# Optimization experiments

Measured on AMD Instinct MI355X. Metric: run time of the kernel, lower is better.

## Reference

```python
import jax, jax.numpy as jnp
import numpy as np

N_VARS = 50_000
N_CLAUSES = 210_000
NNZ = 3 * N_CLAUSES
F = 80
NORM_EPS = 1e-3


def setup_inputs() -> dict:
    key = jax.random.key(0)
    ks = jax.random.split(key, 16)

    def w(k, fan_in, shape):
        return jax.random.normal(k, shape, jnp.float32) * (1.0 / np.sqrt(fan_in))

    inp = {
        'edge_lit': jax.random.randint(ks[0], (NNZ,), 0, 2 * N_VARS, jnp.int32),
        'edge_clause': jnp.sort(jax.random.randint(ks[1], (NNZ,), 0, N_CLAUSES, jnp.int32)),
        'n_vars': N_VARS,
        'n_clauses': N_CLAUSES,
        'L_init_scale': jnp.full((1,), 1.0 / np.sqrt(F), jnp.float32),
        'C_init_scale': jnp.full((1,), 1.0 / np.sqrt(F), jnp.float32),
        'LC_scale': jnp.full((1,), 0.1, jnp.float32),
        'CL_scale': jnp.full((1,), 0.1, jnp.float32),
        # C_update MLP: 160 -> 160 (relu6) -> 80
        'Cw1': w(ks[2], 160, (160, 160)), 'Cb1': jnp.zeros((160,), jnp.float32),
        'Cw2': w(ks[3], 160, (160, 80)), 'Cb2': jnp.zeros((80,), jnp.float32),
        # L_update MLP: 240 -> 240 (relu6) -> 80
        'Lw1': w(ks[4], 240, (240, 240)), 'Lb1': jnp.zeros((240,), jnp.float32),
        'Lw2': w(ks[5], 240, (240, 80)), 'Lb2': jnp.zeros((80,), jnp.float32),
        # V_score MLP: 160 -> 160 -> 160 -> 160 (relu6) -> 1
        'Vw1': w(ks[6], 160, (160, 160)), 'Vb1': jnp.zeros((160,), jnp.float32),
        'Vw2': w(ks[7], 160, (160, 160)), 'Vb2': jnp.zeros((160,), jnp.float32),
        'Vw3': w(ks[8], 160, (160, 160)), 'Vb3': jnp.zeros((160,), jnp.float32),
        'Vw4': w(ks[9], 160, (160, 1)), 'Vb4': jnp.zeros((1,), jnp.float32),
    }
    return inp


def _relu6(x):
    return jnp.minimum(jax.nn.relu(x), 6.0)


def _normalize(x):
    # tf.nn.moments over axis 0 (biased variance) + batch_normalization, no scale/offset
    m = jnp.mean(x, axis=0, keepdims=True)
    v = jnp.var(x, axis=0, keepdims=True)
    return (x - m) / jnp.sqrt(v + NORM_EPS)


def reference(edge_lit, edge_clause, n_vars, n_clauses,
              L_init_scale, C_init_scale, LC_scale, CL_scale,
              Cw1, Cb1, Cw2, Cb2, Lw1, Lb1, Lw2, Lb2,
              Vw1, Vb1, Vw2, Vb2, Vw3, Vb3, Vw4, Vb4):
    n_lits = 2 * n_vars
    L = jnp.ones((n_lits, F), jnp.float32) * L_init_scale
    C = jnp.ones((n_clauses, F), jnp.float32) * C_init_scale

    for _ in range(4):
        # SpMM: adj[n_lits, n_clauses]^T @ L via gather + segment_sum
        LC_msgs = jax.ops.segment_sum(L[edge_lit], edge_clause, num_segments=n_clauses) * LC_scale
        C = _relu6(jnp.concatenate([C, LC_msgs], axis=-1) @ Cw1 + Cb1) @ Cw2 + Cb2
        C = _normalize(C)
        CL_msgs = jax.ops.segment_sum(C[edge_clause], edge_lit, num_segments=n_lits) * CL_scale
        L_flip = jnp.concatenate([L[n_vars:], L[:n_vars]], axis=0)
        L = _relu6(jnp.concatenate([L, CL_msgs, L_flip], axis=-1) @ Lw1 + Lb1) @ Lw2 + Lb2
        L = _normalize(L)

    V = jnp.concatenate([L[:n_vars], L[n_vars:]], axis=1)  # [n_vars, 160]
    h = _relu6(V @ Vw1 + Vb1)
    h = _relu6(h @ Vw2 + Vb2)
    h = _relu6(h @ Vw3 + Vb3)
    V_scores = h @ Vw4 + Vb4  # [n_vars, 1]

    # softplus mixed loss over clauses (edge list encodes signed literals)
    sign = jnp.where(edge_lit < n_vars, 1.0, -1.0).astype(jnp.float32)
    var_idx = jnp.where(edge_lit < n_vars, edge_lit, edge_lit - n_vars)
    lit_vals = V_scores[var_idx, 0] * sign
    clause_sum = jax.ops.segment_sum(jax.nn.softplus(lit_vals), edge_clause, num_segments=n_clauses)
    clauses_val = jnp.exp(-clause_sum)
    logits_loss = jnp.sum(clauses_val * (-jnp.log(1.0 - clauses_val + 1e-8)))
    return V_scores, logits_loss
```

## Files before the change

kernel.cpp:

```cpp
#include <hip/hip_runtime.h>
#include <hip/hip_bf16.h>

#define NV 50000
#define NL 100000
#define NC 210000
#define NNZE 630000
#define F 80

#define TBM 192
#define TBN 80
#define TBK 32
#define LDA 40

#define FBM 128
#define CH 80
#define CHP 96
#define LDH 104

typedef unsigned short us;
typedef __attribute__((ext_vector_type(8))) short s8v;
typedef __attribute__((ext_vector_type(4))) float f4v;
typedef __attribute__((ext_vector_type(4))) unsigned short us4;
typedef __attribute__((ext_vector_type(8))) unsigned short us8;

__device__ inline us bf16_hi(float x) {
    return (us)(__builtin_bit_cast(unsigned int, x) >> 16);
}
__device__ inline float b2f(us h) {
    return __builtin_bit_cast(float, (unsigned int)h << 16);
}

__global__ void build_off(const int* __restrict__ ec, int* __restrict__ off,
                          int nnz, int nc) {
    int e = blockIdx.x * 256 + threadIdx.x;
    if (e >= nnz) return;
    int c = ec[e];
    if (e == 0) {
        for (int cc = 0; cc <= c; ++cc) off[cc] = 0;
    } else {
        int cp = ec[e - 1];
        for (int cc = cp + 1; cc <= c; ++cc) off[cc] = e;
    }
    if (e == nnz - 1) {
        for (int cc = c + 1; cc <= nc; ++cc) off[cc] = nnz;
    }
}

__global__ void fill_val(float* __restrict__ p, int n, const float* __restrict__ v) {
    int i = blockIdx.x * 256 + threadIdx.x;
    if (i < n) p[i] = v[0];
}
__global__ void zero_int(int* __restrict__ p, int n) {
    int i = blockIdx.x * 256 + threadIdx.x;
    if (i < n) p[i] = 0;
}

__global__ void hist_lit(const int* __restrict__ el, int* __restrict__ cnt) {
    int e = blockIdx.x * 256 + threadIdx.x;
    if (e < NNZE) atomicAdd(&cnt[el[e]], 1);
}

__global__ __launch_bounds__(256)
void scan1(const int* __restrict__ cnt, int* __restrict__ bsum, int n) {
    __shared__ int sd[256];
    int i = blockIdx.x * 256 + threadIdx.x;
    sd[threadIdx.x] = (i < n) ? cnt[i] : 0;
    __syncthreads();
    for (int k = 128; k; k >>= 1) {
        if (threadIdx.x < k) sd[threadIdx.x] += sd[threadIdx.x + k];
        __syncthreads();
    }
    if (threadIdx.x == 0) bsum[blockIdx.x] = sd[0];
}

__global__ __launch_bounds__(512)
void scan2(int* __restrict__ bsum, int nb) {
    __shared__ int sd[512];
    int t = threadIdx.x;
    sd[t] = (t < nb) ? bsum[t] : 0;
    __syncthreads();
    for (int off = 1; off < 512; off <<= 1) {
        int v = (t >= off) ? sd[t - off] : 0;
        __syncthreads();
        sd[t] += v;
        __syncthreads();
    }
    if (t < nb) bsum[t] = sd[t];
}

__global__ __launch_bounds__(256)
void scan3(const int* __restrict__ cnt, const int* __restrict__ bsum,
           int* __restrict__ loff, int n) {
    __shared__ int sd[256];
    int t = threadIdx.x;
    int i = blockIdx.x * 256 + t;
    int v = (i < n) ? cnt[i] : 0;
    sd[t] = v;
    __syncthreads();
    for (int off = 1; off < 256; off <<= 1) {
        int u = (t >= off) ? sd[t - off] : 0;
        __syncthreads();
        sd[t] += u;
        __syncthreads();
    }
    int base = blockIdx.x ? bsum[blockIdx.x - 1] : 0;
    if (i < n) loff[i] = base + sd[t] - v;
    if (i == n - 1) loff[n] = base + sd[t];
}

__global__ void scatter_lit(const int* __restrict__ el, const int* __restrict__ ec,
                            const int* __restrict__ loff, int* __restrict__ cur,
                            int* __restrict__ litc) {
    int e = blockIdx.x * 256 + threadIdx.x;
    if (e >= NNZE) return;
    int l = el[e];
    int pos = loff[l] + atomicAdd(&cur[l], 1);
    litc[pos] = ec[e];
}

__global__ void seg_sort(const int* __restrict__ loff, int* __restrict__ litc) {
    int l = blockIdx.x * 256 + threadIdx.x;
    if (l >= NL) return;
    int a = loff[l], b = loff[l + 1];
    for (int i = a + 1; i < b; ++i) {
        int key = litc[i];
        int j = i - 1;
        while (j >= a && litc[j] > key) { litc[j + 1] = litc[j]; --j; }
        litc[j + 1] = key;
    }
}

__global__ void split_w(const float* __restrict__ W, int K, int N,
                        us* __restrict__ Wh, us* __restrict__ Wl) {
    int idx = blockIdx.x * 256 + threadIdx.x;
    if (idx >= K * N) return;
    int k = idx / N, n = idx % N;
    float x = W[idx];
    us h = bf16_hi(x);
    Wh[(size_t)n * K + k] = h;
    Wl[(size_t)n * K + k] = bf16_hi(x - b2f(h));
}

__global__ void lc_gather(const float* __restrict__ L, const int* __restrict__ el,
                          const int* __restrict__ off, const float* __restrict__ scale,
                          float* __restrict__ LC) {
    int idx = blockIdx.x * 256 + threadIdx.x;
    if (idx >= NC * 20) return;
    int c = idx / 20, f4 = idx % 20;
    int e0 = off[c], e1 = off[c + 1];
    float4 s = make_float4(0.f, 0.f, 0.f, 0.f);
    for (int e = e0; e < e1; ++e) {
        const float4 v = *(const float4*)&L[(size_t)el[e] * F + f4 * 4];
        s.x += v.x; s.y += v.y; s.z += v.z; s.w += v.w;
    }
    float sc = scale[0];
    s.x *= sc; s.y *= sc; s.z *= sc; s.w *= sc;
    *(float4*)&LC[(size_t)c * F + f4 * 4] = s;
}

__global__ void cl_gather(const float* __restrict__ C, const int* __restrict__ loff,
                          const int* __restrict__ litc, const float* __restrict__ scale,
                          const float* __restrict__ statsC, float* __restrict__ CL) {
    int idx = blockIdx.x * 256 + threadIdx.x;
    if (idx >= NL * 20) return;
    int lit = idx / 20, f4 = idx % 20;
    int e0 = loff[lit], e1 = loff[lit + 1];
    float4 s = make_float4(0.f, 0.f, 0.f, 0.f);
    for (int e = e0; e < e1; ++e) {
        const float4 v = *(const float4*)&C[(size_t)litc[e] * F + f4 * 4];
        s.x += v.x; s.y += v.y; s.z += v.z; s.w += v.w;
    }
    float sc = scale[0];
    float cnt = (float)(e1 - e0);
    float r[4] = {s.x, s.y, s.z, s.w};
    float4 o;
#pragma unroll
    for (int j = 0; j < 4; ++j) {
        int col = f4 * 4 + j;
        float m = statsC[col], rs = statsC[80 + col];
        r[j] = (r[j] - cnt * m) * rs * sc;
    }
    o.x = r[0]; o.y = r[1]; o.z = r[2]; o.w = r[3];
    *(float4*)&CL[(size_t)lit * F + f4 * 4] = o;
}

__global__ __launch_bounds__(256, 2)
void mlp_fused(const float* __restrict__ A0, const float* __restrict__ A1,
               const float* __restrict__ A2, int pw, int flip2, int rbase,
               int M, int K1, int N1,
               const us* __restrict__ W1h, const us* __restrict__ W1l,
               const float* __restrict__ b1,
               const us* __restrict__ W2h, const us* __restrict__ W2l,
               const float* __restrict__ b2,
               float* __restrict__ Out, const float* __restrict__ nstat,
               float* __restrict__ Psum, float* __restrict__ Psq) {
    __shared__ __align__(16) us AsH[FBM * LDA];
    __shared__ __align__(16) us AsL[FBM * LDA];
    __shared__ __align__(16) us HsH[FBM * LDH];
    __shared__ __align__(16) us HsL[FBM * LDH];
    __shared__ float ns[160];
    __shared__ float bs1[240];
    __shared__ float csum[80], csq[80];

    const int t = threadIdx.x;
    const int m0 = blockIdx.x * FBM;
    const int w = t >> 6;
    const int l = t & 63;
    const int lr = l & 15;
    const int lk = (l >> 4) * 8;
    const int q = t & 3;
    const int rb = t >> 2;

    if (nstat && t < 160) ns[t] = nstat[t];
    if (t < N1) bs1[t] = b1[t];
    if (t < 80) { csum[t] = 0.f; csq[t] = 0.f; }
    for (int u = t; u < FBM * 4; u += 256) {
        int row = u >> 2, cq = u & 3;
        us4 z = {0, 0, 0, 0};
        *(us4*)&HsH[row * LDH + CH + cq * 4] = z;
        *(us4*)&HsL[row * LDH + CH + cq * 4] = z;
    }
    __syncthreads();

    f4v acc2[2][5];
#pragma unroll
    for (int i = 0; i < 2; ++i)
#pragma unroll
        for (int j = 0; j < 5; ++j) acc2[i][j] = (f4v)0.f;

    float4 pa[2][2];

#define ALOAD(K0)                                                              \
    {                                                                          \
        _Pragma("unroll")                                                      \
        for (int i = 0; i < 2; ++i) {                                          \
            int row = m0 + i * 64 + rb;                                        \
            int kg = (K0) + q * 8;                                             \
            float4 z = make_float4(0.f, 0.f, 0.f, 0.f);                        \
            pa[i][0] = z; pa[i][1] = z;                                        \
            if (row < M && kg < K1) {                                          \
                int piece = (kg >= pw) + (kg >= 2 * pw);                       \
                int kk = kg - piece * pw;                                      \
                const float* P = piece == 0 ? A0 : piece == 1 ? A1 : A2;       \
                int re = row;                                                  \
                if (piece == 2 && flip2) {                                     \
                    int g = rbase + row;                                       \
                    re = (g < NV) ? g + NV : g - NV;                           \
                }                                                              \
                const float* src = P + (size_t)re * pw + kk;                   \
                pa[i][0] = *(const float4*)src;                                \
                pa[i][1] = *(const float4*)(src + 4);                          \
                if (piece == 0 && nstat) {                                     \
                    float* pf = (float*)&pa[i][0];                             \
                    _Pragma("unroll")                                          \
                    for (int j = 0; j < 8; ++j)                                \
                        pf[j] = (pf[j] - ns[kk + j]) * ns[80 + kk + j];        \
                }                                                              \
            }                                                                  \
        }                                                                      \
    }

    const int nk1 = (K1 + TBK - 1) / TBK;

    for (int c2 = 0; c2 < N1; c2 += CH) {
        f4v acc1[5][2];
#pragma unroll
        for (int i = 0; i < 5; ++i)
#pragma unroll
            for (int j = 0; j < 2; ++j) acc1[i][j] = (f4v)0.f;

        ALOAD(0);
        for (int s = 0; s < nk1; ++s) {
            const int k0 = s * TBK;
#pragma unroll
            for (int i = 0; i < 2; ++i) {
                float f0[8] = {pa[i][0].x, pa[i][0].y, pa[i][0].z, pa[i][0].w,
                               pa[i][1].x, pa[i][1].y, pa[i][1].z, pa[i][1].w};
                us8 hv, lv;
#pragma unroll
                for (int j = 0; j < 8; ++j) {
                    us h = bf16_hi(f0[j]);
                    hv[j] = h;
                    lv[j] = bf16_hi(f0[j] - b2f(h));
                }
                int r = i * 64 + rb;
                *(us8*)&AsH[r * LDA + q * 8] = hv;
                *(us8*)&AsL[r * LDA + q * 8] = lv;
            }
            __syncthreads();

            s8v aH[2], aL[2], wH[5], wL[5];
#pragma unroll
            for (int mf = 0; mf < 2; ++mf) {
                int ar = w * 32 + mf * 16 + lr;
                aH[mf] = *(const s8v*)&AsH[ar * LDA + lk];
                aL[mf] = *(const s8v*)&AsL[ar * LDA + lk];
            }
            {
                int kg = k0 + lk;
                bool kv = kg < K1;
#pragma unroll
                for (int nf = 0; nf < 5; ++nf) {
                    int br = c2 + nf * 16 + lr;
                    s8v z = {0, 0, 0, 0, 0, 0, 0, 0};
                    wH[nf] = kv ? *(const s8v*)&W1h[(size_t)br * K1 + kg] : z;
                    wL[nf] = kv ? *(const s8v*)&W1l[(size_t)br * K1 + kg] : z;
                }
            }
            if (s + 1 < nk1) ALOAD(k0 + TBK);
#pragma unroll
            for (int nf = 0; nf < 5; ++nf)
#pragma unroll
                for (int mf = 0; mf < 2; ++mf) {
                    acc1[nf][mf] = __builtin_amdgcn_mfma_f32_16x16x32_bf16(wH[nf], aH[mf], acc1[nf][mf], 0, 0, 0);
                    acc1[nf][mf] = __builtin_amdgcn_mfma_f32_16x16x32_bf16(wL[nf], aH[mf], acc1[nf][mf], 0, 0, 0);
                    acc1[nf][mf] = __builtin_amdgcn_mfma_f32_16x16x32_bf16(wH[nf], aL[mf], acc1[nf][mf], 0, 0, 0);
                }
            __syncthreads();
        }

#pragma unroll
        for (int nf = 0; nf < 5; ++nf) {
            int n1b = nf * 16 + ((l >> 4) << 2);
#pragma unroll
            for (int mf = 0; mf < 2; ++mf) {
                int m = w * 32 + mf * 16 + lr;
                us4 hv, lv;
#pragma unroll
                for (int r = 0; r < 4; ++r) {
                    float v = acc1[nf][mf][r] + bs1[c2 + n1b + r];
                    v = fminf(fmaxf(v, 0.f), 6.f);
                    us h = bf16_hi(v);
                    hv[r] = h;
                    lv[r] = bf16_hi(v - b2f(h));
                }
                *(us4*)&HsH[m * LDH + n1b] = hv;
                *(us4*)&HsL[m * LDH + n1b] = lv;
            }
        }
        __syncthreads();

#pragma unroll
        for (int ks = 0; ks < 3; ++ks) {
            int klocal = ks * 32 + lk;
            s8v a2H[2], a2L[2], b2H[5], b2L[5];
#pragma unroll
            for (int mf = 0; mf < 2; ++mf) {
                int ar = w * 32 + mf * 16 + lr;
                a2H[mf] = *(const s8v*)&HsH[ar * LDH + klocal];
                a2L[mf] = *(const s8v*)&HsL[ar * LDH + klocal];
            }
            bool bval = klocal < CH;
            int kg = c2 + klocal;
#pragma unroll
            for (int nf = 0; nf < 5; ++nf) {
                int n2 = nf * 16 + lr;
                s8v z = {0, 0, 0, 0, 0, 0, 0, 0};
                b2H[nf] = bval ? *(const s8v*)&W2h[(size_t)n2 * N1 + kg] : z;
                b2L[nf] = bval ? *(const s8v*)&W2l[(size_t)n2 * N1 + kg] : z;
            }
#pragma unroll
            for (int mf = 0; mf < 2; ++mf)
#pragma unroll
                for (int nf = 0; nf < 5; ++nf) {
                    acc2[mf][nf] = __builtin_amdgcn_mfma_f32_16x16x32_bf16(a2H[mf], b2H[nf], acc2[mf][nf], 0, 0, 0);
                    acc2[mf][nf] = __builtin_amdgcn_mfma_f32_16x16x32_bf16(a2L[mf], b2H[nf], acc2[mf][nf], 0, 0, 0);
                    acc2[mf][nf] = __builtin_amdgcn_mfma_f32_16x16x32_bf16(a2H[mf], b2L[nf], acc2[mf][nf], 0, 0, 0);
                }
        }
        __syncthreads();
    }
#undef ALOAD

#pragma unroll
    for (int nf = 0; nf < 5; ++nf) {
        int col = nf * 16 + lr;
        float bv = b2[col];
        float ls = 0.f, lq = 0.f;
#pragma unroll
        for (int mf = 0; mf < 2; ++mf) {
            int rowb = m0 + w * 32 + mf * 16 + (l >> 4) * 4;
#pragma unroll
            for (int r = 0; r < 4; ++r) {
                int row = rowb + r;
                if (row < M) {
                    float v = acc2[mf][nf][r] + bv;
                    Out[(size_t)row * 80 + col] = v;
                    ls += v; lq += v * v;
                }
            }
        }
        ls += __shfl_xor(ls, 16); ls += __shfl_xor(ls, 32);
        lq += __shfl_xor(lq, 16); lq += __shfl_xor(lq, 32);
        if (l < 16) {
            atomicAdd(&csum[col], ls);
            atomicAdd(&csq[col], lq);
        }
    }
    __syncthreads();
    if (t < 80) {
        size_t pb = (size_t)blockIdx.x * 80 + t;
        Psum[pb] = csum[t];
        Psq[pb] = csq[t];
    }
}

__global__ __launch_bounds__(256, 3)
void gemm_mfma(const float* __restrict__ A0, const float* __restrict__ A1,
               const float* __restrict__ A2, int pw, int flip2, int rbase,
               int M, int K, int N,
               const us* __restrict__ Wh, const us* __restrict__ Wl,
               const float* __restrict__ bias, float* __restrict__ Out, int act) {
    __shared__ __align__(16) us AsH[TBM * LDA];
    __shared__ __align__(16) us AsL[TBM * LDA];
    __shared__ __align__(16) us BsH[TBN * LDA];
    __shared__ __align__(16) us BsL[TBN * LDA];

    const int t = threadIdx.x;
    const int m0 = blockIdx.x * TBM;
    const int n0 = blockIdx.y * TBN;
    const int w = t >> 6;
    const int l = t & 63;
    const int lr = l & 15;
    const int lk = (l >> 4) * 8;
    const int q = t & 3;
    const int rb = t >> 2;

    f4v acc[3][5];
#pragma unroll
    for (int i = 0; i < 3; ++i)
#pragma unroll
        for (int j = 0; j < 5; ++j) acc[i][j] = (f4v)0.f;

    float4 pa[3][2];

#define ALOAD(K0)                                                              \
    {                                                                          \
        _Pragma("unroll")                                                      \
        for (int i = 0; i < 3; ++i) {                                          \
            int row = m0 + i * 64 + rb;                                        \
            int kg = (K0) + q * 8;                                             \
            float4 z = make_float4(0.f, 0.f, 0.f, 0.f);                        \
            pa[i][0] = z; pa[i][1] = z;                                        \
            if (row < M && kg < K) {                                           \
                int piece = (kg >= pw) + (kg >= 2 * pw);                       \
                int kk = kg - piece * pw;                                      \
                const float* P = piece == 0 ? A0 : piece == 1 ? A1 : A2;       \
                int re = row;                                                  \
                if (piece == 2 && flip2) {                                     \
                    int g = rbase + row;                                       \
                    re = (g < NV) ? g + NV : g - NV;                           \
                }                                                              \
                const float* src = P + (size_t)re * pw + kk;                   \
                pa[i][0] = *(const float4*)src;                                \
                pa[i][1] = *(const float4*)(src + 4);                          \
            }                                                                  \
        }                                                                      \
    }

    const int nk = (K + TBK - 1) / TBK;
    ALOAD(0);

    for (int s = 0; s < nk; ++s) {
        const int k0 = s * TBK;
#pragma unroll
        for (int i = 0; i < 3; ++i) {
            float f0[8] = {pa[i][0].x, pa[i][0].y, pa[i][0].z, pa[i][0].w,
                           pa[i][1].x, pa[i][1].y, pa[i][1].z, pa[i][1].w};
            us8 hv, lv;
#pragma unroll
            for (int j = 0; j < 8; ++j) {
                us h = bf16_hi(f0[j]);
                hv[j] = h;
                lv[j] = bf16_hi(f0[j] - b2f(h));
            }
            int r = i * 64 + rb;
            *(us8*)&AsH[r * LDA + q * 8] = hv;
            *(us8*)&AsL[r * LDA + q * 8] = lv;
        }
#pragma unroll
        for (int i = 0; i < 3; ++i) {
            int u = i * 256 + t;
            if (u < 640) {
                int hi = (u < 320);
                int c = hi ? u : u - 320;
                int n = c >> 2, cq = c & 3;
                int kg = k0 + cq * 8;
                us8 v = {0, 0, 0, 0, 0, 0, 0, 0};
                if (kg < K)
                    v = *(const us8*)&(hi ? Wh : Wl)[(size_t)(n0 + n) * K + kg];
                *(us8*)&(hi ? BsH : BsL)[n * LDA + cq * 8] = v;
            }
        }
        __syncthreads();

        s8v aH[3], aL[3], bH[5], bL[5];
#pragma unroll
        for (int mf = 0; mf < 3; ++mf) {
            int ar = w * 48 + mf * 16 + lr;
            aH[mf] = *(const s8v*)&AsH[ar * LDA + lk];
            aL[mf] = *(const s8v*)&AsL[ar * LDA + lk];
        }
#pragma unroll
        for (int nf = 0; nf < 5; ++nf) {
            int br = nf * 16 + lr;
            bH[nf] = *(const s8v*)&BsH[br * LDA + lk];
            bL[nf] = *(const s8v*)&BsL[br * LDA + lk];
        }
        if (s + 1 < nk) ALOAD(k0 + TBK);
#pragma unroll
        for (int mf = 0; mf < 3; ++mf)
#pragma unroll
            for (int nf = 0; nf < 5; ++nf) {
                acc[mf][nf] = __builtin_amdgcn_mfma_f32_16x16x32_bf16(aH[mf], bH[nf], acc[mf][nf], 0, 0, 0);
                acc[mf][nf] = __builtin_amdgcn_mfma_f32_16x16x32_bf16(aL[mf], bH[nf], acc[mf][nf], 0, 0, 0);
                acc[mf][nf] = __builtin_amdgcn_mfma_f32_16x16x32_bf16(aH[mf], bL[nf], acc[mf][nf], 0, 0, 0);
            }
        __syncthreads();
    }
#undef ALOAD

#pragma unroll
    for (int mf = 0; mf < 3; ++mf) {
        int rowb = m0 + w * 48 + mf * 16 + (l >> 4) * 4;
#pragma unroll
        for (int nf = 0; nf < 5; ++nf) {
            int col = n0 + nf * 16 + lr;
            float bv = bias[col];
#pragma unroll
            for (int r = 0; r < 4; ++r) {
                int row = rowb + r;
                if (row < M) {
                    float v = acc[mf][nf][r] + bv;
                    if (act) v = fminf(fmaxf(v, 0.f), 6.f);
                    Out[(size_t)row * N + col] = v;
                }
            }
        }
    }
}

__global__ __launch_bounds__(256)
void colstats_final(const float* __restrict__ Psum, const float* __restrict__ Psq,
                    int nblk, int M, float* __restrict__ stats) {
    __shared__ float sd[256], qd[256];
    int c = blockIdx.x;
    int tid = threadIdx.x;
    float s = 0.f, q = 0.f;
    for (int b = tid; b < nblk; b += 256) {
        s += Psum[(size_t)b * 80 + c];
        q += Psq [(size_t)b * 80 + c];
    }
    sd[tid] = s; qd[tid] = q;
    __syncthreads();
    for (int k = 128; k; k >>= 1) {
        if (tid < k) { sd[tid] += sd[tid + k]; qd[tid] += qd[tid + k]; }
        __syncthreads();
    }
    if (tid == 0) {
        float mean = sd[0] / (float)M;
        float var = qd[0] / (float)M - mean * mean;
        if (var < 0.f) var = 0.f;
        stats[c] = mean;
        stats[80 + c] = rsqrtf(var + 1e-3f);
    }
}

__global__ void norm_apply(float* __restrict__ X, int M, const float* __restrict__ stats) {
    int idx = blockIdx.x * 256 + threadIdx.x;
    if (idx >= M * F) return;
    int c = idx % F;
    X[idx] = (X[idx] - stats[c]) * stats[80 + c];
}

__global__ __launch_bounds__(256)
void vscore_kernel(const float* __restrict__ H, const float* __restrict__ w,
                   const float* __restrict__ b, float* __restrict__ out, int M) {
    int wid = (blockIdx.x * 256 + threadIdx.x) / 64;
    int lane = threadIdx.x % 64;
    if (wid >= M) return;
    const float* row = H + (size_t)wid * 160;
    float s = 0.f;
    for (int c = lane; c < 160; c += 64) s += row[c] * w[c];
    for (int off = 32; off; off >>= 1) s += __shfl_down(s, off);
    if (lane == 0) out[wid] = s + b[0];
}

__global__ __launch_bounds__(256)
void loss_clause(const int* __restrict__ el, const int* __restrict__ off,
                 const float* __restrict__ scores, float* __restrict__ partial, int nc) {
    __shared__ float sd[256];
    int c = blockIdx.x * 256 + threadIdx.x;
    float term = 0.f;
    if (c < nc) {
        int e0 = off[c], e1 = off[c + 1];
        float cs = 0.f;
        for (int e = e0; e < e1; ++e) {
            int lit = el[e];
            float v = (lit < NV) ? scores[lit] : -scores[lit - NV];
            cs += fmaxf(v, 0.f) + log1pf(expf(-fabsf(v)));
        }
        float cv = expf(-cs);
        term = cv * (-logf(1.0f - cv + 1e-8f));
    }
    sd[threadIdx.x] = term;
    __syncthreads();
    for (int s = 128; s; s >>= 1) {
        if (threadIdx.x < s) sd[threadIdx.x] += sd[threadIdx.x + s];
        __syncthreads();
    }
    if (threadIdx.x == 0) partial[blockIdx.x] = sd[0];
}

__global__ void loss_final(const float* __restrict__ partial, int n, float* __restrict__ out) {
    __shared__ float sd[256];
    float s = 0.f;
    for (int i = threadIdx.x; i < n; i += 256) s += partial[i];
    sd[threadIdx.x] = s;
    __syncthreads();
    for (int k = 128; k; k >>= 1) {
        if (threadIdx.x < k) sd[threadIdx.x] += sd[threadIdx.x + k];
        __syncthreads();
    }
    if (threadIdx.x == 0) out[0] = sd[0];
}

static inline size_t alignup(size_t x) { return (x + 255) & ~(size_t)255; }

extern "C" void kernel_launch(void* const* d_in, const int* in_sizes, int n_in,
                              void* d_out, int out_size, void* d_ws, size_t ws_size,
                              hipStream_t stream) {
    const int*   el   = (const int*)d_in[0];
    const int*   ec   = (const int*)d_in[1];
    const float* l_init = (const float*)d_in[4];
    const float* c_init = (const float*)d_in[5];
    const float* lc_s = (const float*)d_in[6];
    const float* cl_s = (const float*)d_in[7];
    const float* Cw1 = (const float*)d_in[8],  *Cb1 = (const float*)d_in[9];
    const float* Cw2 = (const float*)d_in[10], *Cb2 = (const float*)d_in[11];
    const float* Lw1 = (const float*)d_in[12], *Lb1 = (const float*)d_in[13];
    const float* Lw2 = (const float*)d_in[14], *Lb2 = (const float*)d_in[15];
    const float* Vw1 = (const float*)d_in[16], *Vb1 = (const float*)d_in[17];
    const float* Vw2 = (const float*)d_in[18], *Vb2 = (const float*)d_in[19];
    const float* Vw3 = (const float*)d_in[20], *Vb3 = (const float*)d_in[21];
    const float* Vw4 = (const float*)d_in[22], *Vb4 = (const float*)d_in[23];
    float* out = (float*)d_out;

    char* p = (char*)d_ws;
    size_t o = 0;
    int* off  = (int*)(p + o); o += alignup((size_t)(NC + 1) * 4);
    int* loff = (int*)(p + o); o += alignup((size_t)(NL + 1) * 4);
    int* lcnt = (int*)(p + o); o += alignup((size_t)NL * 4);
    int* lcur = (int*)(p + o); o += alignup((size_t)NL * 4);
    int* bsum = (int*)(p + o); o += alignup((size_t)512 * 4);
    int* litc = (int*)(p + o); o += alignup((size_t)NNZE * 4);
    float* L0  = (float*)(p + o); o += alignup((size_t)NL * F * 4);
    float* L1  = (float*)(p + o); o += alignup((size_t)NL * F * 4);
    float* Cb  = (float*)(p + o); o += alignup((size_t)NC * F * 4);
    float* MSG = (float*)(p + o); o += alignup((size_t)NC * F * 4);
    float* H   = (float*)(p + o); o += alignup((size_t)8400000 * 4);
    float* Psum = (float*)(p + o); o += alignup((size_t)2048 * 80 * 4);
    float* Psq  = (float*)(p + o); o += alignup((size_t)2048 * 80 * 4);
    float* statsC = (float*)(p + o); o += alignup(160 * 4);
    float* statsL = (float*)(p + o); o += alignup(160 * 4);
    float* lossP  = (float*)(p + o); o += alignup(1024 * 4);
    us* Wsp = (us*)(p + o); o += alignup((size_t)192000 * 2 * 2);
    us* Cw1h = Wsp,          *Cw1l = Cw1h + 25600;
    us* Cw2h = Cw1l + 25600, *Cw2l = Cw2h + 12800;
    us* Lw1h = Cw2l + 12800, *Lw1l = Lw1h + 57600;
    us* Lw2h = Lw1l + 57600, *Lw2l = Lw2h + 19200;
    us* Vw1h = Lw2l + 19200, *Vw1l = Vw1h + 25600;
    us* Vw2h = Vw1l + 25600, *Vw2l = Vw2h + 25600;
    us* Vw3h = Vw2l + 25600, *Vw3l = Vw3h + 25600;
    (void)ws_size; (void)n_in; (void)in_sizes; (void)out_size;

    build_off<<<(NNZE + 255) / 256, 256, 0, stream>>>(ec, off, NNZE, NC);
    zero_int<<<(NL + 255) / 256, 256, 0, stream>>>(lcnt, NL);
    zero_int<<<(NL + 255) / 256, 256, 0, stream>>>(lcur, NL);
    hist_lit<<<(NNZE + 255) / 256, 256, 0, stream>>>(el, lcnt);
    const int nb = (NL + 255) / 256;
    scan1<<<nb, 256, 0, stream>>>(lcnt, bsum, NL);
    scan2<<<1, 512, 0, stream>>>(bsum, nb);
    scan3<<<nb, 256, 0, stream>>>(lcnt, bsum, loff, NL);
    scatter_lit<<<(NNZE + 255) / 256, 256, 0, stream>>>(el, ec, loff, lcur, litc);
    seg_sort<<<(NL + 255) / 256, 256, 0, stream>>>(loff, litc);

    split_w<<<(25600 + 255) / 256, 256, 0, stream>>>(Cw1, 160, 160, Cw1h, Cw1l);
    split_w<<<(12800 + 255) / 256, 256, 0, stream>>>(Cw2, 160,  80, Cw2h, Cw2l);
    split_w<<<(57600 + 255) / 256, 256, 0, stream>>>(Lw1, 240, 240, Lw1h, Lw1l);
    split_w<<<(19200 + 255) / 256, 256, 0, stream>>>(Lw2, 240,  80, Lw2h, Lw2l);
    split_w<<<(25600 + 255) / 256, 256, 0, stream>>>(Vw1, 160, 160, Vw1h, Vw1l);
    split_w<<<(25600 + 255) / 256, 256, 0, stream>>>(Vw2, 160, 160, Vw2h, Vw2l);
    split_w<<<(25600 + 255) / 256, 256, 0, stream>>>(Vw3, 160, 160, Vw3h, Vw3l);

    fill_val<<<(NL * F + 255) / 256, 256, 0, stream>>>(L0, NL * F, l_init);
    fill_val<<<(NC * F + 255) / 256, 256, 0, stream>>>(Cb, NC * F, c_init);

    float* Lc = L0, *Ln = L1;
    const int nblkC = (NC + FBM - 1) / FBM;
    const int nblkL = (NL + FBM - 1) / FBM;

    for (int round = 0; round < 4; ++round) {
        float* LC = MSG;
        lc_gather<<<(NC * 20 + 255) / 256, 256, 0, stream>>>(Lc, el, off, lc_s, LC);

        const float* nsC = (round > 0) ? statsC : nullptr;
        mlp_fused<<<nblkC, 256, 0, stream>>>(Cb, LC, nullptr, 80, 0, 0, NC, 160, 160,
                                             Cw1h, Cw1l, Cb1, Cw2h, Cw2l, Cb2,
                                             Cb, nsC, Psum, Psq);
        colstats_final<<<80, 256, 0, stream>>>(Psum, Psq, nblkC, NC, statsC);

        float* CL = MSG;
        cl_gather<<<(NL * 20 + 255) / 256, 256, 0, stream>>>(Cb, loff, litc, cl_s, statsC, CL);

        mlp_fused<<<nblkL, 256, 0, stream>>>(Lc, CL, Lc, 80, 1, 0, NL, 240, 240,
                                             Lw1h, Lw1l, Lb1, Lw2h, Lw2l, Lb2,
                                             Ln, nullptr, Psum, Psq);
        colstats_final<<<80, 256, 0, stream>>>(Psum, Psq, nblkL, NL, statsL);
        norm_apply<<<(NL * F + 255) / 256, 256, 0, stream>>>(Ln, NL, statsL);

        float* t = Lc; Lc = Ln; Ln = t;
    }

    {
        float* H2 = MSG;
        dim3 g((NV + TBM - 1) / TBM, 2);
        gemm_mfma<<<g, 256, 0, stream>>>(Lc, Lc + (size_t)NV * F, nullptr, 80, 0, 0,
                                         NV, 160, 160, Vw1h, Vw1l, Vb1, H, 1);
        gemm_mfma<<<g, 256, 0, stream>>>(H, nullptr, nullptr, 160, 0, 0,
                                         NV, 160, 160, Vw2h, Vw2l, Vb2, H2, 1);
        gemm_mfma<<<g, 256, 0, stream>>>(H2, nullptr, nullptr, 160, 0, 0,
                                         NV, 160, 160, Vw3h, Vw3l, Vb3, H, 1);
        vscore_kernel<<<(NV * 64 + 255) / 256, 256, 0, stream>>>(H, Vw4, Vb4, out, NV);
    }

    {
        int nblk = (NC + 255) / 256;
        loss_clause<<<nblk, 256, 0, stream>>>(el, off, out, lossP, NC);
        loss_final<<<1, 256, 0, stream>>>(lossP, nblk, out + NV);
    }
}
```

Measured before the change: 1.807 ms.

## Load MLP A fragments directly from global into registers, dropping LDS staging

The fused MLP kernel no longer stages the input activation tile through shared memory. Each wave now loads, normalizes and splits into bf16 hi/lo pairs only the rows it consumes, straight into MFMA operand registers. Because every wave reads and writes only its own rows of the hidden buffer, all block-wide barriers are removed. This cuts LDS traffic, barrier stalls and shared-memory footprint, which may allow higher occupancy. In exchange it gives up the register prefetch of the next K slice, so global load latency is less hidden.

New measurement: 1.825 ms. About the same (+1.0%).

```diff
diff --git a/kernel.cpp b/kernel.cpp
--- a/kernel.cpp
+++ b/kernel.cpp
@@ -14,7 +14,6 @@
 
 #define FBM 128
 #define CH 80
-#define CHP 96
 #define LDH 104
 
 typedef unsigned short us;
@@ -194,8 +193,6 @@
                const float* __restrict__ b2,
                float* __restrict__ Out, const float* __restrict__ nstat,
                float* __restrict__ Psum, float* __restrict__ Psq) {
-    __shared__ __align__(16) us AsH[FBM * LDA];
-    __shared__ __align__(16) us AsL[FBM * LDA];
     __shared__ __align__(16) us HsH[FBM * LDH];
     __shared__ __align__(16) us HsL[FBM * LDH];
     __shared__ float ns[160];
@@ -208,8 +205,6 @@
     const int l = t & 63;
     const int lr = l & 15;
     const int lk = (l >> 4) * 8;
-    const int q = t & 3;
-    const int rb = t >> 2;
 
     if (nstat && t < 160) ns[t] = nstat[t];
     if (t < N1) bs1[t] = b1[t];
@@ -228,38 +223,6 @@
 #pragma unroll
         for (int j = 0; j < 5; ++j) acc2[i][j] = (f4v)0.f;
 
-    float4 pa[2][2];
-
-#define ALOAD(K0)                                                              \
-    {                                                                          \
-        _Pragma("unroll")                                                      \
-        for (int i = 0; i < 2; ++i) {                                          \
-            int row = m0 + i * 64 + rb;                                        \
-            int kg = (K0) + q * 8;                                             \
-            float4 z = make_float4(0.f, 0.f, 0.f, 0.f);                        \
-            pa[i][0] = z; pa[i][1] = z;                                        \
-            if (row < M && kg < K1) {                                          \
-                int piece = (kg >= pw) + (kg >= 2 * pw);                       \
-                int kk = kg - piece * pw;                                      \
-                const float* P = piece == 0 ? A0 : piece == 1 ? A1 : A2;       \
-                int re = row;                                                  \
-                if (piece == 2 && flip2) {                                     \
-                    int g = rbase + row;                                       \
-                    re = (g < NV) ? g + NV : g - NV;                           \
-                }                                                              \
-                const float* src = P + (size_t)re * pw + kk;                   \
-                pa[i][0] = *(const float4*)src;                                \
-                pa[i][1] = *(const float4*)(src + 4);                          \
-                if (piece == 0 && nstat) {                                     \
-                    float* pf = (float*)&pa[i][0];                             \
-                    _Pragma("unroll")                                          \
-                    for (int j = 0; j < 8; ++j)                                \
-                        pf[j] = (pf[j] - ns[kk + j]) * ns[80 + kk + j];        \
-                }                                                              \
-            }                                                                  \
-        }                                                                      \
-    }
-
     const int nk1 = (K1 + TBK - 1) / TBK;
 
     for (int c2 = 0; c2 < N1; c2 += CH) {
@@ -269,45 +232,51 @@
 #pragma unroll
             for (int j = 0; j < 2; ++j) acc1[i][j] = (f4v)0.f;
 
-        ALOAD(0);
         for (int s = 0; s < nk1; ++s) {
-            const int k0 = s * TBK;
-#pragma unroll
-            for (int i = 0; i < 2; ++i) {
-                float f0[8] = {pa[i][0].x, pa[i][0].y, pa[i][0].z, pa[i][0].w,
-                               pa[i][1].x, pa[i][1].y, pa[i][1].z, pa[i][1].w};
-                us8 hv, lv;
-#pragma unroll
-                for (int j = 0; j < 8; ++j) {
-                    us h = bf16_hi(f0[j]);
-                    hv[j] = h;
-                    lv[j] = bf16_hi(f0[j] - b2f(h));
+            const int kg = s * TBK + lk;
+            const bool kv = kg < K1;
+
+            s8v aH[2], aL[2];
+#pragma unroll
+            for (int mf = 0; mf < 2; ++mf) {
+                s8v h8 = {0, 0, 0, 0, 0, 0, 0, 0};
+                s8v l8 = {0, 0, 0, 0, 0, 0, 0, 0};
+                int row = m0 + w * 32 + mf * 16 + lr;
+                if (kv && row < M) {
+                    int piece = (kg >= pw) + (kg >= 2 * pw);
+                    int kk = kg - piece * pw;
+                    const float* P = piece == 0 ? A0 : piece == 1 ? A1 : A2;
+                    int re = row;
+                    if (piece == 2 && flip2) {
+                        int g = rbase + row;
+                        re = (g < NV) ? g + NV : g - NV;
+                    }
+                    const float* src = P + (size_t)re * pw + kk;
+                    float4 v0 = *(const float4*)src;
+                    float4 v1 = *(const float4*)(src + 4);
+                    float f0[8] = {v0.x, v0.y, v0.z, v0.w, v1.x, v1.y, v1.z, v1.w};
+                    if (piece == 0 && nstat) {
+#pragma unroll
+                        for (int j = 0; j < 8; ++j)
+                            f0[j] = (f0[j] - ns[kk + j]) * ns[80 + kk + j];
+                    }
+#pragma unroll
+                    for (int j = 0; j < 8; ++j) {
+                        us h = bf16_hi(f0[j]);
+                        h8[j] = (short)h;
+                        l8[j] = (short)bf16_hi(f0[j] - b2f(h));
+                    }
                 }
-                int r = i * 64 + rb;
-                *(us8*)&AsH[r * LDA + q * 8] = hv;
-                *(us8*)&AsL[r * LDA + q * 8] = lv;
-            }
-            __syncthreads();
-
-            s8v aH[2], aL[2], wH[5], wL[5];
-#pragma unroll
-            for (int mf = 0; mf < 2; ++mf) {
-                int ar = w * 32 + mf * 16 + lr;
-                aH[mf] = *(const s8v*)&AsH[ar * LDA + lk];
-                aL[mf] = *(const s8v*)&AsL[ar * LDA + lk];
-            }
-            {
-                int kg = k0 + lk;
-                bool kv = kg < K1;
-#pragma unroll
-                for (int nf = 0; nf < 5; ++nf) {
-                    int br = c2 + nf * 16 + lr;
-                    s8v z = {0, 0, 0, 0, 0, 0, 0, 0};
-                    wH[nf] = kv ? *(const s8v*)&W1h[(size_t)br * K1 + kg] : z;
-                    wL[nf] = kv ? *(const s8v*)&W1l[(size_t)br * K1 + kg] : z;
-                }
-            }
-            if (s + 1 < nk1) ALOAD(k0 + TBK);
+                aH[mf] = h8; aL[mf] = l8;
+            }
+            s8v wH[5], wL[5];
+#pragma unroll
+            for (int nf = 0; nf < 5; ++nf) {
+                int br = c2 + nf * 16 + lr;
+                s8v z = {0, 0, 0, 0, 0, 0, 0, 0};
+                wH[nf] = kv ? *(const s8v*)&W1h[(size_t)br * K1 + kg] : z;
+                wL[nf] = kv ? *(const s8v*)&W1l[(size_t)br * K1 + kg] : z;
+            }
 #pragma unroll
             for (int nf = 0; nf < 5; ++nf)
 #pragma unroll
@@ -316,7 +285,6 @@
                     acc1[nf][mf] = __builtin_amdgcn_mfma_f32_16x16x32_bf16(wL[nf], aH[mf], acc1[nf][mf], 0, 0, 0);
                     acc1[nf][mf] = __builtin_amdgcn_mfma_f32_16x16x32_bf16(wH[nf], aL[mf], acc1[nf][mf], 0, 0, 0);
                 }
-            __syncthreads();
         }
 
 #pragma unroll
@@ -338,7 +306,6 @@
                 *(us4*)&HsL[m * LDH + n1b] = lv;
             }
         }
-        __syncthreads();
 
 #pragma unroll
         for (int ks = 0; ks < 3; ++ks) {
@@ -368,9 +335,7 @@
                     acc2[mf][nf] = __builtin_amdgcn_mfma_f32_16x16x32_bf16(a2H[mf], b2L[nf], acc2[mf][nf], 0, 0, 0);
                 }
         }
-        __syncthreads();
-    }
-#undef ALOAD
+    }
 
 #pragma unroll
     for (int nf = 0; nf < 5; ++nf) {
```
